# Optimization experiments

Hardware: AMD Instinct MI355X
Metric: run time of the kernel (lower is better)

## Reference

```python
import jax, jax.numpy as jnp
import numpy as np
import math

B, S, D, H = 16, 1024, 768, 12
Dh = D // H  # 64


def setup_inputs() -> dict:
    key = jax.random.key(0)
    ks = jax.random.split(key, 9)
    scale = 1.0 / math.sqrt(D)
    X = jax.random.normal(ks[0], (B, S, D), dtype=jnp.float32)
    # Per-head Q/K/V projections stacked along head dim: [H, D, Dh]
    Wq = jax.random.normal(ks[1], (H, D, Dh), dtype=jnp.float32) * scale
    Wk = jax.random.normal(ks[2], (H, D, Dh), dtype=jnp.float32) * scale
    Wv = jax.random.normal(ks[3], (H, D, Dh), dtype=jnp.float32) * scale
    bq = jax.random.normal(ks[4], (H, Dh), dtype=jnp.float32) * scale
    bk = jax.random.normal(ks[5], (H, Dh), dtype=jnp.float32) * scale
    bv = jax.random.normal(ks[6], (H, Dh), dtype=jnp.float32) * scale
    Wo = jax.random.normal(ks[7], (D, D), dtype=jnp.float32) * scale
    bo = jax.random.normal(ks[8], (D,), dtype=jnp.float32) * scale
    return {"X": X, "Wq": Wq, "bq": bq, "Wk": Wk, "bk": bk,
            "Wv": Wv, "bv": bv, "Wo": Wo, "bo": bo}


def reference(X, Wq, bq, Wk, bk, Wv, bv, Wo, bo):
    # Batched multi-head QKV projections (equivalent to the per-head Linear loop).
    Q = jnp.einsum('bsd,hde->bhse', X, Wq) + bq[None, :, None, :]
    K = jnp.einsum('bsd,hde->bhse', X, Wk) + bk[None, :, None, :]
    V = jnp.einsum('bsd,hde->bhse', X, Wv) + bv[None, :, None, :]
    scores = jnp.einsum('bhse,bhte->bhst', Q, K) / jnp.sqrt(jnp.float32(Dh))
    A = jax.nn.softmax(scores, axis=-1)            # [B,H,S,S]
    O = jnp.einsum('bhst,bhte->bhse', A, V)        # [B,H,S,Dh]
    # Concat heads along feature dim (matches torch cat order: head 0 first).
    msa = jnp.transpose(O, (0, 2, 1, 3)).reshape(B, S, D)
    return msa @ Wo + bo
```

## Files before the change

kernel.cpp:

```cpp
#include <hip/hip_runtime.h>
#include <hip/hip_bf16.h>

#define BB 16
#define SS 1024
#define DD 768
#define HH 12
#define DH 64

typedef short short8 __attribute__((ext_vector_type(8)));
typedef float f32x4 __attribute__((ext_vector_type(4)));

__device__ inline float b2f(unsigned short v) {
    union { unsigned int u; float f; } x; x.u = ((unsigned int)v) << 16; return x.f;
}
__device__ inline unsigned short f2b(float f) {
    unsigned int u = __float_as_uint(f);
    u += 0x7FFFu + ((u >> 16) & 1u);
    return (unsigned short)(u >> 16);
}
__device__ inline unsigned int pk2(float a, float b) {
    __hip_bfloat162 h = __float22bfloat162_rn(make_float2(a, b));
    return *(unsigned int*)&h;
}
__device__ __forceinline__ float fast_exp2(float x) {
#if __has_builtin(__builtin_amdgcn_exp2f)
    return __builtin_amdgcn_exp2f(x);
#else
    return exp2f(x);
#endif
}
__device__ inline void cvt8(unsigned short* dst, const float* src) {
    const float4 f0 = *(const float4*)src;
    const float4 f1 = *(const float4*)(src + 4);
    unsigned short t[8] = {f2b(f0.x), f2b(f0.y), f2b(f0.z), f2b(f0.w),
                           f2b(f1.x), f2b(f1.y), f2b(f1.z), f2b(f1.w)};
    *(uint4*)dst = *(const uint4*)t;
}
__device__ __forceinline__ void async16(const void* g, void* l) {
    __builtin_amdgcn_global_load_lds(
        (const __attribute__((address_space(1))) void*)g,
        (__attribute__((address_space(3))) void*)l, 16, 0, 0);
}

__global__ __launch_bounds__(256) void detect_kernel(const unsigned short* __restrict__ X,
                                                     int* __restrict__ flag) {
    __shared__ int s;
    if (threadIdx.x == 0) s = 0;
    __syncthreads();
    int c = 0;
    for (int i = threadIdx.x; i < 16384; i += 256) {
        unsigned short v = X[i];
        if ((v & 0x7FFFu) >= 0x7F80u) c = 1;
    }
    if (c) s = 1;
    __syncthreads();
    if (threadIdx.x == 0) flag[0] = s;
}

__global__ __launch_bounds__(256) void prep_all(
    const void* __restrict__ Xv,
    const void* __restrict__ Wqv, const void* __restrict__ bqv,
    const void* __restrict__ Wkv, const void* __restrict__ bkv,
    const void* __restrict__ Wvv, const void* __restrict__ bvv,
    const void* __restrict__ Wov, const void* __restrict__ bov,
    const int* __restrict__ flag,
    unsigned short* __restrict__ Xb, unsigned short* __restrict__ Wc,
    unsigned short* __restrict__ Wot, unsigned short* __restrict__ bc,
    float* __restrict__ bo32)
{
    __shared__ unsigned short Ls[64][72];
    const int dt = *flag;
    const int u = threadIdx.x;
    const int bx = blockIdx.x;

    if (bx < 6144) {
        size_t base = ((size_t)bx * 256 + u) * 8;
        if (dt) cvt8(Xb + base, (const float*)Xv + base);
        else    *(uint4*)(Xb + base) = *(const uint4*)((const unsigned short*)Xv + base);
        return;
    }
    if (bx < 6720) {
        const int idx = bx - 6144;
        const int kt = idx % 12;
        const int y  = idx / 12;
        const int rk = u >> 2;
        const int e0 = (u & 3) * 16;

        const void* src; size_t srcBase;
        unsigned short* dst; int drow;
        if (y < 36) {
            int z = y / 12, h = y % 12;
            src = (z == 0) ? Wqv : (z == 1) ? Wkv : Wvv;
            srcBase = ((size_t)h * DD + kt * 64 + rk) * DH;
            dst = Wc; drow = z * 768 + h * 64;
        } else {
            int nt = y - 36;
            src = Wov;
            srcBase = (size_t)(kt * 64 + rk) * DD + nt * 64;
            dst = Wot; drow = nt * 64;
        }
#pragma unroll
        for (int ii = 0; ii < 2; ++ii) {
            int e = e0 + ii * 8;
            if (dt) {
                const float* p = (const float*)src + srcBase + e;
                float4 a = *(const float4*)p, b = *(const float4*)(p + 4);
                float v[8] = {a.x, a.y, a.z, a.w, b.x, b.y, b.z, b.w};
#pragma unroll
                for (int j = 0; j < 8; ++j) Ls[e + j][rk] = f2b(v[j]);
            } else {
                union { uint4 v; unsigned short s[8]; } t;
                t.v = *(const uint4*)((const unsigned short*)src + srcBase + e);
#pragma unroll
                for (int j = 0; j < 8; ++j) Ls[e + j][rk] = t.s[j];
            }
        }
        __syncthreads();
        const int e = u >> 2, q = u & 3;
#pragma unroll
        for (int ii = 0; ii < 2; ++ii) {
            int kk = q * 16 + ii * 8;
            *(uint4*)(dst + (size_t)(drow + e) * DD + kt * 64 + kk) = *(const uint4*)(&Ls[e][kk]);
        }
        return;
    }
    for (int n = u; n < 2304; n += 256) {
        int z = n / 768, i = n % 768;
        const void* b = (z == 0) ? bqv : (z == 1) ? bkv : bvv;
        bc[n] = dt ? f2b(((const float*)b)[i]) : ((const unsigned short*)b)[i];
    }
    for (int n = u; n < 768; n += 256)
        bo32[n] = dt ? ((const float*)bov)[n] : b2f(((const unsigned short*)bov)[n]);
}

__global__ __launch_bounds__(256) void qkv_gemm(
    const unsigned short* __restrict__ Xb,
    const unsigned short* __restrict__ Wc,
    const unsigned short* __restrict__ bc,
    unsigned short* __restrict__ Qb, unsigned short* __restrict__ Kb,
    unsigned short* __restrict__ Vtb)
{
    __shared__ __align__(16) unsigned short lds[17408];
    unsigned short* As = lds;
    unsigned short* Bs = lds + 128 * 64;

    const int u = threadIdx.x;
    const int lane = u & 63, w = u >> 6;
    const int ln = lane & 15, quad = lane >> 4;
    const int wm = w & 1, wn = w >> 1;

    const int nt0 = blockIdx.x;
    const int m0  = blockIdx.y << 7;
    const int n0  = nt0 << 7;
    const int z   = nt0 / 6;
    const int hpair = (nt0 % 6) * 2;

    const int rA = w * 32 + (lane >> 3);
    const int c8 = (((lane & 7) ^ (lane >> 3)) * 8);

    f32x4 acc[4][4];
#pragma unroll
    for (int i = 0; i < 4; ++i)
#pragma unroll
        for (int j = 0; j < 4; ++j) acc[i][j] = (f32x4){0.f, 0.f, 0.f, 0.f};

    const unsigned short* Ag = Xb + (size_t)(m0 + rA) * DD + c8;
    const unsigned short* Bg = Wc + (size_t)(n0 + rA) * DD + c8;
    unsigned short* lA0 = As + w * 2048;
    unsigned short* lB0 = Bs + w * 2048;

    for (int kb = 0; kb < 12; ++kb) {
        const int k0 = kb * 64;
        if (kb) __syncthreads();
#pragma unroll
        for (int j = 0; j < 4; ++j) {
            async16(Ag + (size_t)j * 8 * DD + k0, lA0 + j * 512);
            async16(Bg + (size_t)j * 8 * DD + k0, lB0 + j * 512);
        }
        __syncthreads();
#pragma unroll
        for (int kh = 0; kh < 2; ++kh) {
            const int sx = ((kh * 4 + quad) ^ (ln & 7)) * 8;
            short8 af[4], bf[4];
#pragma unroll
            for (int t = 0; t < 4; ++t) {
                af[t] = *(const short8*)(As + (wm * 64 + t * 16 + ln) * 64 + sx);
                bf[t] = *(const short8*)(Bs + (wn * 64 + t * 16 + ln) * 64 + sx);
            }
#pragma unroll
            for (int mt = 0; mt < 4; ++mt)
#pragma unroll
                for (int nt = 0; nt < 4; ++nt)
                    acc[mt][nt] = __builtin_amdgcn_mfma_f32_16x16x32_bf16(af[mt], bf[nt], acc[mt][nt], 0, 0, 0);
        }
    }

    float bias[4];
#pragma unroll
    for (int nt = 0; nt < 4; ++nt) bias[nt] = b2f(bc[n0 + wn * 64 + nt * 16 + ln]);

    const int b = m0 >> 10;
    if (z < 2) {
        unsigned short* O = (z == 0) ? Qb : Kb;
        const float sc = (z == 0) ? 0.180336880111120f : 1.0f;
        const int h = hpair + wn;
        const int sb = (m0 & 1023) + wm * 64;
#pragma unroll
        for (int mt = 0; mt < 4; ++mt)
#pragma unroll
            for (int r = 0; r < 4; ++r) {
                int s = sb + mt * 16 + quad * 4 + r;
                size_t rowo = ((size_t)(b * HH + h) * SS + s) * DH;
#pragma unroll
                for (int nt = 0; nt < 4; ++nt)
                    O[rowo + nt * 16 + ln] = f2b((acc[mt][nt][r] + bias[nt]) * sc);
            }
    } else {
        __syncthreads();
#pragma unroll
        for (int mt = 0; mt < 4; ++mt)
#pragma unroll
            for (int nt = 0; nt < 4; ++nt)
#pragma unroll
                for (int r = 0; r < 4; ++r)
                    lds[(wn * 64 + nt * 16 + ln) * 136 + wm * 64 + mt * 16 + quad * 4 + r] =
                        f2b(acc[mt][nt][r] + bias[nt]);
        __syncthreads();
        const int cc = u >> 1, half = u & 1;
        const int h = hpair + (cc >> 6), e = cc & 63;
        const int sb = (m0 & 1023) + half * 64;
        unsigned short* dst = Vtb + ((size_t)(b * HH + h) * DH + e) * SS + sb;
        const unsigned short* srcp = lds + cc * 136 + half * 64;
#pragma unroll
        for (int i = 0; i < 8; ++i)
            *(uint4*)(dst + i * 8) = *(const uint4*)(srcp + i * 8);
    }
}

__global__ __launch_bounds__(256, 4) void attn_kernel(
    const unsigned short* __restrict__ Kb,
    const unsigned short* __restrict__ Vtb,
    unsigned short* __restrict__ Qb)
{
    __shared__ __align__(16) unsigned short QPs[8192];
    __shared__ __align__(16) unsigned short Ks[4096];
    __shared__ __align__(16) unsigned short Vs[4096];

    const int u = threadIdx.x;
    const int s0 = blockIdx.x << 7;
    const int bh = blockIdx.y;

    const int lane = u & 63, w = u >> 6;
    const int ln = lane & 15, quad = lane >> 4;

    unsigned short* Qg = Qb + ((size_t)bh * SS + s0) * DH;
    const unsigned short* Kg = Kb + (size_t)bh * SS * DH;
    const unsigned short* Vg = Vtb + (size_t)bh * DH * SS;

    const int srow = lane >> 3;
    const int cg8  = ((lane & 7) ^ srow) * 8;

#pragma unroll
    for (int j = 0; j < 4; ++j) {
        const int r0 = (w * 4 + j) * 8 + srow;
        async16(Qg + (size_t)r0 * DH + cg8, QPs + (w * 4 + j) * 512);
    }
    __syncthreads();

    short8 qf[2][2];
#pragma unroll
    for (int b = 0; b < 2; ++b) {
        const int rb = b * 64 + 16 * w + ln;
#pragma unroll
        for (int kh = 0; kh < 2; ++kh)
            qf[b][kh] = *(const short8*)(QPs + rb * 64 + ((kh * 4 + quad) ^ (ln & 7)) * 8);
    }

    short8 ones;
#pragma unroll
    for (int i = 0; i < 8; ++i) ones[i] = (short)0x3F80;

    f32x4 acc_o[2][4];
#pragma unroll
    for (int b = 0; b < 2; ++b)
#pragma unroll
        for (int i = 0; i < 4; ++i) acc_o[b][i] = (f32x4){0.f, 0.f, 0.f, 0.f};
    f32x4 acc_l[2];
    acc_l[0] = (f32x4){0.f, 0.f, 0.f, 0.f};
    acc_l[1] = (f32x4){0.f, 0.f, 0.f, 0.f};

    const unsigned short* kp0 = Kg + (size_t)((w * 2 + 0) * 8 + srow) * DH + cg8;
    const unsigned short* kp1 = Kg + (size_t)((w * 2 + 1) * 8 + srow) * DH + cg8;
    const unsigned short* vp0 = Vg + (size_t)((w * 2 + 0) * 8 + srow) * SS + cg8;
    const unsigned short* vp1 = Vg + (size_t)((w * 2 + 1) * 8 + srow) * SS + cg8;
    unsigned short* lk0 = Ks + (w * 2 + 0) * 512;
    unsigned short* lk1 = Ks + (w * 2 + 1) * 512;
    unsigned short* lv0 = Vs + (w * 2 + 0) * 512;
    unsigned short* lv1 = Vs + (w * 2 + 1) * 512;

    const unsigned short* kb0 = Ks + ln * 64 + ((quad ^ (ln & 7)) * 8);
    const unsigned short* kb1 = Ks + ln * 64 + (((4 + quad) ^ (ln & 7)) * 8);
    const unsigned short* vb0 = Vs + ln * 64 + ((quad ^ (ln & 7)) * 8);
    const unsigned short* vb1 = Vs + ln * 64 + (((4 + quad) ^ (ln & 7)) * 8);

    for (int kt = 0; kt < 16; ++kt) {
        __syncthreads();
        async16(kp0, lk0); async16(kp1, lk1);
        async16(vp0, lv0); async16(vp1, lv1);
        kp0 += 64 * DH; kp1 += 64 * DH; vp0 += 64; vp1 += 64;
        __syncthreads();

        f32x4 acc_s[2][4];
#pragma unroll
        for (int nt = 0; nt < 4; ++nt) {
            short8 kf0 = *(const short8*)(kb0 + nt * 1024);
            short8 kf1 = *(const short8*)(kb1 + nt * 1024);
#pragma unroll
            for (int b = 0; b < 2; ++b) {
                f32x4 zz = (f32x4){0.f, 0.f, 0.f, 0.f};
                zz = __builtin_amdgcn_mfma_f32_16x16x32_bf16(kf0, qf[b][0], zz, 0, 0, 0);
                zz = __builtin_amdgcn_mfma_f32_16x16x32_bf16(kf1, qf[b][1], zz, 0, 0, 0);
                acc_s[b][nt] = zz;
            }
        }

#pragma unroll
        for (int b = 0; b < 2; ++b) {
            unsigned short* pb = QPs + (b * 64 + 16 * w + ln) * 64 + (quad & 1) * 4;
#pragma unroll
            for (int nt = 0; nt < 4; ++nt) {
                uint2 pw;
                pw.x = pk2(fast_exp2(acc_s[b][nt][0]), fast_exp2(acc_s[b][nt][1]));
                pw.y = pk2(fast_exp2(acc_s[b][nt][2]), fast_exp2(acc_s[b][nt][3]));
                const int c = (nt * 2 + (quad >> 1)) ^ (ln & 7);
                *(uint2*)(pb + c * 8) = pw;
            }
        }

        short8 pf[2][2];
#pragma unroll
        for (int b = 0; b < 2; ++b) {
            const unsigned short* pr = QPs + (b * 64 + 16 * w + ln) * 64;
            pf[b][0] = *(const short8*)(pr + ((quad ^ (ln & 7)) * 8));
            pf[b][1] = *(const short8*)(pr + (((4 + quad) ^ (ln & 7)) * 8));
            acc_l[b] = __builtin_amdgcn_mfma_f32_16x16x32_bf16(pf[b][0], ones, acc_l[b], 0, 0, 0);
            acc_l[b] = __builtin_amdgcn_mfma_f32_16x16x32_bf16(pf[b][1], ones, acc_l[b], 0, 0, 0);
        }
#pragma unroll
        for (int nt = 0; nt < 4; ++nt) {
            short8 vf0 = *(const short8*)(vb0 + nt * 1024);
            short8 vf1 = *(const short8*)(vb1 + nt * 1024);
#pragma unroll
            for (int b = 0; b < 2; ++b) {
                acc_o[b][nt] = __builtin_amdgcn_mfma_f32_16x16x32_bf16(pf[b][0], vf0, acc_o[b][nt], 0, 0, 0);
                acc_o[b][nt] = __builtin_amdgcn_mfma_f32_16x16x32_bf16(pf[b][1], vf1, acc_o[b][nt], 0, 0, 0);
            }
        }
    }

#pragma unroll
    for (int b = 0; b < 2; ++b) {
        float inv[4];
#pragma unroll
        for (int r = 0; r < 4; ++r) inv[r] = 1.f / acc_l[b][r];
#pragma unroll
        for (int nt = 0; nt < 4; ++nt)
#pragma unroll
            for (int r = 0; r < 4; ++r) {
                int row = b * 64 + 16 * w + quad * 4 + r;
                Qg[row * DH + nt * 16 + ln] = f2b(acc_o[b][nt][r] * inv[r]);
            }
    }
}

__global__ __launch_bounds__(256) void oproj_gemm(
    const unsigned short* __restrict__ Ob,
    const unsigned short* __restrict__ Wot,
    const float* __restrict__ bo32,
    float* __restrict__ out)
{
    __shared__ __align__(16) unsigned short lds[128 * 128];
    unsigned short* As = lds;
    unsigned short* Bs = lds + 128 * 64;

    const int u = threadIdx.x;
    const int lane = u & 63, w = u >> 6;
    const int ln = lane & 15, quad = lane >> 4;
    const int wm = w & 1, wn = w >> 1;

    const int n0 = blockIdx.x << 7;
    const int m0 = blockIdx.y << 7;
    const int b = m0 >> 10, s0t = m0 & 1023;

    const int rA = w * 32 + (lane >> 3);
    const int c8 = (((lane & 7) ^ (lane >> 3)) * 8);

    f32x4 acc[4][4];
#pragma unroll
    for (int i = 0; i < 4; ++i)
#pragma unroll
        for (int j = 0; j < 4; ++j) acc[i][j] = (f32x4){0.f, 0.f, 0.f, 0.f};

    const unsigned short* Bg = Wot + (size_t)(n0 + rA) * DD + c8;
    unsigned short* lA0 = As + w * 2048;
    unsigned short* lB0 = Bs + w * 2048;

    for (int kb = 0; kb < 12; ++kb) {
        if (kb) __syncthreads();
        const unsigned short* Ag = Ob + ((size_t)(b * HH + kb) * SS + s0t + rA) * DH + c8;
#pragma unroll
        for (int j = 0; j < 4; ++j) {
            async16(Ag + (size_t)j * 8 * DH, lA0 + j * 512);
            async16(Bg + (size_t)j * 8 * DD + kb * 64, lB0 + j * 512);
        }
        __syncthreads();
#pragma unroll
        for (int kh = 0; kh < 2; ++kh) {
            const int sx = ((kh * 4 + quad) ^ (ln & 7)) * 8;
            short8 af[4], bf[4];
#pragma unroll
            for (int t = 0; t < 4; ++t) {
                af[t] = *(const short8*)(As + (wm * 64 + t * 16 + ln) * 64 + sx);
                bf[t] = *(const short8*)(Bs + (wn * 64 + t * 16 + ln) * 64 + sx);
            }
#pragma unroll
            for (int mt = 0; mt < 4; ++mt)
#pragma unroll
                for (int nt = 0; nt < 4; ++nt)
                    acc[mt][nt] = __builtin_amdgcn_mfma_f32_16x16x32_bf16(af[mt], bf[nt], acc[mt][nt], 0, 0, 0);
        }
    }

    float bias[4];
#pragma unroll
    for (int nt = 0; nt < 4; ++nt) bias[nt] = bo32[n0 + wn * 64 + nt * 16 + ln];
#pragma unroll
    for (int mt = 0; mt < 4; ++mt)
#pragma unroll
        for (int r = 0; r < 4; ++r) {
            int m = m0 + wm * 64 + mt * 16 + quad * 4 + r;
            float* orow = out + (size_t)m * DD + n0 + wn * 64;
#pragma unroll
            for (int nt = 0; nt < 4; ++nt)
                orow[nt * 16 + ln] = acc[mt][nt][r] + bias[nt];
        }
}

extern "C" void kernel_launch(void* const* d_in, const int* in_sizes, int n_in,
                              void* d_out, int out_size, void* d_ws, size_t ws_size,
                              hipStream_t stream)
{
    const void* X  = d_in[0];
    const void* Wq = d_in[1];
    const void* bq = d_in[2];
    const void* Wk = d_in[3];
    const void* bk = d_in[4];
    const void* Wv = d_in[5];
    const void* bv = d_in[6];
    const void* Wo = d_in[7];
    const void* bo = d_in[8];
    float* out = (float*)d_out;

    const size_t NE = (size_t)BB * HH * SS * DH;
    char* p = (char*)d_ws;
    int* flag = (int*)p;                 p += 256;
    unsigned short* Qb  = (unsigned short*)p;  p += NE * 2;
    unsigned short* Kb  = (unsigned short*)p;  p += NE * 2;
    unsigned short* Vtb = (unsigned short*)p;  p += NE * 2;
    unsigned short* Xb  = (unsigned short*)p;  p += (size_t)BB * SS * DD * 2;
    unsigned short* Wc  = (unsigned short*)p;  p += (size_t)3 * DD * DD * 2;
    unsigned short* Wot = (unsigned short*)p;  p += (size_t)DD * DD * 2;
    unsigned short* bcb = (unsigned short*)p;  p += 4608;
    float* bo32 = (float*)p;                   p += 3072;

    detect_kernel<<<1, 256, 0, stream>>>((const unsigned short*)X, flag);
    prep_all<<<6721, 256, 0, stream>>>(X, Wq, bq, Wk, bk, Wv, bv, Wo, bo, flag,
                                       Xb, Wc, Wot, bcb, bo32);
    qkv_gemm<<<dim3(18, 128), 256, 0, stream>>>(Xb, Wc, bcb, Qb, Kb, Vtb);
    attn_kernel<<<dim3(8, 192), 256, 0, stream>>>(Kb, Vtb, Qb);
    oproj_gemm<<<dim3(6, 128), 256, 0, stream>>>(Qb, Wot, bo32, out);
}
```

Baseline: 300.8 us.

## Double-buffer K/V tiles in attention and remap blocks for XCD-local reuse

Attention now keeps two LDS buffers each for K and V. The next tile's async loads are issued before computing on the current tile, so the two barriers per iteration drop to one. Block indices are permuted so that blocks landing on the same XCD share a batch-head, which should improve L2 reuse of K/V. LDS use grows and the occupancy hint falls from 4 to 3 blocks per CU, which may hurt latency hiding.

```diff
diff --git a/kernel.cpp b/kernel.cpp
--- a/kernel.cpp
+++ b/kernel.cpp
@@ -237,18 +237,20 @@
     }
 }
 
-__global__ __launch_bounds__(256, 4) void attn_kernel(
+__global__ __launch_bounds__(256, 3) void attn_kernel(
     const unsigned short* __restrict__ Kb,
     const unsigned short* __restrict__ Vtb,
     unsigned short* __restrict__ Qb)
 {
     __shared__ __align__(16) unsigned short QPs[8192];
-    __shared__ __align__(16) unsigned short Ks[4096];
-    __shared__ __align__(16) unsigned short Vs[4096];
+    __shared__ __align__(16) unsigned short Ks[2][4096];
+    __shared__ __align__(16) unsigned short Vs[2][4096];
 
     const int u = threadIdx.x;
-    const int s0 = blockIdx.x << 7;
-    const int bh = blockIdx.y;
+    const int flat = (blockIdx.y << 3) | blockIdx.x;
+    const int swz  = (flat & 7) * 192 + (flat >> 3);
+    const int s0 = (swz & 7) << 7;
+    const int bh = swz >> 3;
 
     const int lane = u & 63, w = u >> 6;
     const int ln = lane & 15, quad = lane >> 4;
@@ -260,11 +262,21 @@
     const int srow = lane >> 3;
     const int cg8  = ((lane & 7) ^ srow) * 8;
 
+    const unsigned short* kp0 = Kg + (size_t)((w * 2 + 0) * 8 + srow) * DH + cg8;
+    const unsigned short* kp1 = Kg + (size_t)((w * 2 + 1) * 8 + srow) * DH + cg8;
+    const unsigned short* vp0 = Vg + (size_t)((w * 2 + 0) * 8 + srow) * SS + cg8;
+    const unsigned short* vp1 = Vg + (size_t)((w * 2 + 1) * 8 + srow) * SS + cg8;
+
 #pragma unroll
     for (int j = 0; j < 4; ++j) {
         const int r0 = (w * 4 + j) * 8 + srow;
         async16(Qg + (size_t)r0 * DH + cg8, QPs + (w * 4 + j) * 512);
     }
+    async16(kp0, &Ks[0][(w * 2 + 0) * 512]);
+    async16(kp1, &Ks[0][(w * 2 + 1) * 512]);
+    async16(vp0, &Vs[0][(w * 2 + 0) * 512]);
+    async16(vp1, &Vs[0][(w * 2 + 1) * 512]);
+    kp0 += 64 * DH; kp1 += 64 * DH; vp0 += 64; vp1 += 64;
     __syncthreads();
 
     short8 qf[2][2];
@@ -289,32 +301,29 @@
     acc_l[0] = (f32x4){0.f, 0.f, 0.f, 0.f};
     acc_l[1] = (f32x4){0.f, 0.f, 0.f, 0.f};
 
-    const unsigned short* kp0 = Kg + (size_t)((w * 2 + 0) * 8 + srow) * DH + cg8;
-    const unsigned short* kp1 = Kg + (size_t)((w * 2 + 1) * 8 + srow) * DH + cg8;
-    const unsigned short* vp0 = Vg + (size_t)((w * 2 + 0) * 8 + srow) * SS + cg8;
-    const unsigned short* vp1 = Vg + (size_t)((w * 2 + 1) * 8 + srow) * SS + cg8;
-    unsigned short* lk0 = Ks + (w * 2 + 0) * 512;
-    unsigned short* lk1 = Ks + (w * 2 + 1) * 512;
-    unsigned short* lv0 = Vs + (w * 2 + 0) * 512;
-    unsigned short* lv1 = Vs + (w * 2 + 1) * 512;
-
-    const unsigned short* kb0 = Ks + ln * 64 + ((quad ^ (ln & 7)) * 8);
-    const unsigned short* kb1 = Ks + ln * 64 + (((4 + quad) ^ (ln & 7)) * 8);
-    const unsigned short* vb0 = Vs + ln * 64 + ((quad ^ (ln & 7)) * 8);
-    const unsigned short* vb1 = Vs + ln * 64 + (((4 + quad) ^ (ln & 7)) * 8);
+    const unsigned short* kb0 = &Ks[0][0] + ln * 64 + ((quad ^ (ln & 7)) * 8);
+    const unsigned short* kb1 = &Ks[0][0] + ln * 64 + (((4 + quad) ^ (ln & 7)) * 8);
+    const unsigned short* vb0 = &Vs[0][0] + ln * 64 + ((quad ^ (ln & 7)) * 8);
+    const unsigned short* vb1 = &Vs[0][0] + ln * 64 + (((4 + quad) ^ (ln & 7)) * 8);
 
     for (int kt = 0; kt < 16; ++kt) {
-        __syncthreads();
-        async16(kp0, lk0); async16(kp1, lk1);
-        async16(vp0, lv0); async16(vp1, lv1);
-        kp0 += 64 * DH; kp1 += 64 * DH; vp0 += 64; vp1 += 64;
-        __syncthreads();
+        const int cur = kt & 1;
+        if (kt < 15) {
+            unsigned short* lk = &Ks[cur ^ 1][(w * 2) * 512];
+            unsigned short* lv = &Vs[cur ^ 1][(w * 2) * 512];
+            async16(kp0, lk);
+            async16(kp1, lk + 512);
+            async16(vp0, lv);
+            async16(vp1, lv + 512);
+            kp0 += 64 * DH; kp1 += 64 * DH; vp0 += 64; vp1 += 64;
+        }
+        const int cb = cur * 4096;
 
         f32x4 acc_s[2][4];
 #pragma unroll
         for (int nt = 0; nt < 4; ++nt) {
-            short8 kf0 = *(const short8*)(kb0 + nt * 1024);
-            short8 kf1 = *(const short8*)(kb1 + nt * 1024);
+            short8 kf0 = *(const short8*)(kb0 + cb + nt * 1024);
+            short8 kf1 = *(const short8*)(kb1 + cb + nt * 1024);
 #pragma unroll
             for (int b = 0; b < 2; ++b) {
                 f32x4 zz = (f32x4){0.f, 0.f, 0.f, 0.f};
@@ -348,14 +357,15 @@
         }
 #pragma unroll
         for (int nt = 0; nt < 4; ++nt) {
-            short8 vf0 = *(const short8*)(vb0 + nt * 1024);
-            short8 vf1 = *(const short8*)(vb1 + nt * 1024);
+            short8 vf0 = *(const short8*)(vb0 + cb + nt * 1024);
+            short8 vf1 = *(const short8*)(vb1 + cb + nt * 1024);
 #pragma unroll
             for (int b = 0; b < 2; ++b) {
                 acc_o[b][nt] = __builtin_amdgcn_mfma_f32_16x16x32_bf16(pf[b][0], vf0, acc_o[b][nt], 0, 0, 0);
                 acc_o[b][nt] = __builtin_amdgcn_mfma_f32_16x16x32_bf16(pf[b][1], vf1, acc_o[b][nt], 0, 0, 0);
             }
         }
+        __syncthreads();
     }
 
 #pragma unroll
```

After: 292.9 us. -2.6%, faster.
